# Kernel optimization log

Hardware: AMD Instinct MI355X
Metric: run time of the kernel (lower is better)

The kernel has to match this reference:

```python
import jax, jax.numpy as jnp
import numpy as np
from jax import lax

TAU = 2.0
V_TH = 1.0
V_RESET = 0.0
ALPHA = 2.0

@jax.custom_vjp
def atan_spike(u):
    # Heaviside forward, ATan surrogate backward
    return (u >= 0).astype(u.dtype)

def _atan_fwd(u):
    return atan_spike(u), u

def _atan_bwd(u, g):
    grad = (ALPHA / 2.0) / (1.0 + (ALPHA * jnp.pi / 2.0 * u) ** 2)
    return (g * grad,)

atan_spike.defvjp(_atan_fwd, _atan_bwd)


def setup_inputs() -> dict:
    key = jax.random.key(0)
    k1, k2 = jax.random.split(key)
    T, B, C_in, H, Wd = 8, 16, 64, 64, 64
    C_out = 128
    x = jax.random.normal(k1, (T, B, C_in, H, Wd), dtype=jnp.float32)
    # kaiming-like scale for 3x3 conv
    W = jax.random.normal(k2, (C_out, C_in, 3, 3), dtype=jnp.float32) * (1.0 / np.sqrt(C_in * 9))
    return {"x": x, "W": W}


def reference(x, W):
    T, B, C_in, H, Wd = x.shape
    C_out = W.shape[0]
    # conv over flattened (T*B) batch, 3x3, padding=1, no bias
    z = lax.conv_general_dilated(
        x.reshape(T * B, C_in, H, Wd), W,
        window_strides=(1, 1), padding="SAME",
        dimension_numbers=("NCHW", "OIHW", "NCHW"))
    z = z.reshape(T, B, C_out, H, Wd)

    def step(v, xt):
        # v_reset = 0: v += (x - v) / tau
        v = v + (xt - (v - V_RESET)) / TAU
        s = atan_spike(v - V_TH)
        v = v * (1.0 - s) + V_RESET * s
        return v, s

    _, spikes = lax.scan(step, jnp.zeros_like(z[0]), z)
    return spikes  # [T, B, C_out, H, W]
```

## Files before the change

### kernel.cpp

```cpp
#include <hip/hip_runtime.h>

#define TT 8
#define BB 16
#define CIN 64
#define COUT 128
#define HH 64
#define WW 64

#define TILE_H 4
#define TILE_W 16
#define XS_H (TILE_H + 2)
#define XS_W (TILE_W + 2)
#define XS_ROW (XS_H * XS_W)
#define XS_N (CIN * XS_ROW)

__global__ __launch_bounds__(256, 2)
void convlif_f64(const float* __restrict__ x, const float* __restrict__ Wt,
                 float* __restrict__ out) {
    __shared__ double xs[XS_N];

    const int tid = threadIdx.x;
    const int pt = tid & 15;
    const int cg = tid >> 4;
    const int w0 = blockIdx.x * TILE_W;
    const int h0 = blockIdx.y * TILE_H;
    const int b = blockIdx.z;
    const int co_base = cg * 8;

    double v[32];
#pragma unroll
    for (int i = 0; i < 32; ++i) v[i] = 0.0;

    for (int t = 0; t < TT; ++t) {
        __syncthreads();
        const float* xb = x + (size_t)(t * BB + b) * (CIN * HH * WW);
        for (int idx = tid; idx < XS_N; idx += 256) {
            int ci = idx / XS_ROW;
            int rem = idx - ci * XS_ROW;
            int hh = rem / XS_W;
            int ww2 = rem - hh * XS_W;
            int gh = h0 - 1 + hh;
            int gw = w0 - 1 + ww2;
            double val = 0.0;
            if (gh >= 0 && gh < HH && gw >= 0 && gw < WW)
                val = (double)xb[ci * (HH * WW) + gh * WW + gw];
            xs[idx] = val;
        }
        __syncthreads();

        double acc[32];
#pragma unroll
        for (int i = 0; i < 32; ++i) acc[i] = 0.0;

        for (int ci = 0; ci < CIN; ++ci) {
            const float* wr = Wt + (size_t)co_base * (CIN * 9) + ci * 9;
            const double* xr = xs + ci * XS_ROW;
#pragma unroll
            for (int kh = 0; kh < 3; ++kh) {
#pragma unroll
                for (int kw = 0; kw < 3; ++kw) {
                    double wv[8];
#pragma unroll
                    for (int i = 0; i < 8; ++i)
                        wv[i] = (double)wr[i * (CIN * 9) + kh * 3 + kw];
                    double xv[4];
#pragma unroll
                    for (int j = 0; j < 4; ++j)
                        xv[j] = xr[(j + kh) * XS_W + pt + kw];
#pragma unroll
                    for (int i = 0; i < 8; ++i) {
#pragma unroll
                        for (int j = 0; j < 4; ++j)
                            acc[i * 4 + j] = fma(wv[i], xv[j], acc[i * 4 + j]);
                    }
                }
            }
        }

        float* ob = out + (size_t)(t * BB + b) * (COUT * HH * WW);
#pragma unroll
        for (int i = 0; i < 8; ++i) {
#pragma unroll
            for (int j = 0; j < 4; ++j) {
                int k = i * 4 + j;
                double vv = v[k] + (acc[k] - v[k]) * 0.5;
                bool s = (vv >= 1.0);
                ob[(size_t)(co_base + i) * (HH * WW) + (h0 + j) * WW + (w0 + pt)]
                    = s ? 1.0f : 0.0f;
                v[k] = s ? 0.0 : vv;
            }
        }
    }
}

extern "C" void kernel_launch(void* const* d_in, const int* in_sizes, int n_in,
                              void* d_out, int out_size, void* d_ws, size_t ws_size,
                              hipStream_t stream) {
    const float* x = (const float*)d_in[0];
    const float* Wt = (const float*)d_in[1];
    float* out = (float*)d_out;
    dim3 grid(WW / TILE_W, HH / TILE_H, BB);
    convlif_f64<<<grid, 256, 0, stream>>>(x, Wt, out);
}
```

Measured before the change: 2.271 ms.

## Pre-convert weights to transposed fp64 and chunk input channels in LDS

A new prepass kernel converts the fp32 weights into an fp64 array in the workspace, transposed so the 8 output channels a thread needs are contiguous and can be read as double2 vector loads. Per-FMA float-to-double conversion and strided weight loads are removed. The input-channel loop is split into chunks of 32, which halves the LDS tile so three blocks can fit per CU (launch bounds raised to 3). This adds an extra kernel launch and two more barriers per timestep. The old kernel is kept as a fallback for when the workspace is too small.

Result: slower. 3.437 ms (+51.3%).

```diff
diff --git a/kernel.cpp b/kernel.cpp
--- a/kernel.cpp
+++ b/kernel.cpp
@@ -12,11 +12,25 @@
 #define XS_H (TILE_H + 2)
 #define XS_W (TILE_W + 2)
 #define XS_ROW (XS_H * XS_W)
-#define XS_N (CIN * XS_ROW)
-
-__global__ __launch_bounds__(256, 2)
-void convlif_f64(const float* __restrict__ x, const float* __restrict__ Wt,
-                 float* __restrict__ out) {
+#define CI_CHUNK 32
+#define XS_N (CI_CHUNK * XS_ROW)
+
+#define W_ELEMS (CIN * 9 * COUT)
+#define W_BYTES (W_ELEMS * 8)
+
+__global__ void wconv_f64(const float* __restrict__ Wt, double* __restrict__ wd) {
+    int idx = blockIdx.x * 256 + threadIdx.x;
+    if (idx >= W_ELEMS) return;
+    int co = idx & 127;
+    int cik = idx >> 7;
+    int ci = cik / 9;
+    int k = cik - ci * 9;
+    wd[idx] = (double)Wt[((size_t)co * CIN + ci) * 9 + k];
+}
+
+__global__ __launch_bounds__(256, 3)
+void convlif_f64w(const float* __restrict__ x, const double* __restrict__ wd,
+                  float* __restrict__ out) {
     __shared__ double xs[XS_N];
 
     const int tid = threadIdx.x;
@@ -32,37 +46,37 @@
     for (int i = 0; i < 32; ++i) v[i] = 0.0;
 
     for (int t = 0; t < TT; ++t) {
-        __syncthreads();
         const float* xb = x + (size_t)(t * BB + b) * (CIN * HH * WW);
-        for (int idx = tid; idx < XS_N; idx += 256) {
-            int ci = idx / XS_ROW;
-            int rem = idx - ci * XS_ROW;
-            int hh = rem / XS_W;
-            int ww2 = rem - hh * XS_W;
-            int gh = h0 - 1 + hh;
-            int gw = w0 - 1 + ww2;
-            double val = 0.0;
-            if (gh >= 0 && gh < HH && gw >= 0 && gw < WW)
-                val = (double)xb[ci * (HH * WW) + gh * WW + gw];
-            xs[idx] = val;
-        }
-        __syncthreads();
-
         double acc[32];
 #pragma unroll
         for (int i = 0; i < 32; ++i) acc[i] = 0.0;
 
-        for (int ci = 0; ci < CIN; ++ci) {
-            const float* wr = Wt + (size_t)co_base * (CIN * 9) + ci * 9;
-            const double* xr = xs + ci * XS_ROW;
-#pragma unroll
-            for (int kh = 0; kh < 3; ++kh) {
-#pragma unroll
-                for (int kw = 0; kw < 3; ++kw) {
-                    double wv[8];
-#pragma unroll
-                    for (int i = 0; i < 8; ++i)
-                        wv[i] = (double)wr[i * (CIN * 9) + kh * 3 + kw];
+        for (int cc = 0; cc < CIN; cc += CI_CHUNK) {
+            __syncthreads();
+            for (int idx = tid; idx < XS_N; idx += 256) {
+                int cil = idx / XS_ROW;
+                int rem = idx - cil * XS_ROW;
+                int hh = rem / XS_W;
+                int ww2 = rem - hh * XS_W;
+                int gh = h0 - 1 + hh;
+                int gw = w0 - 1 + ww2;
+                double val = 0.0;
+                if (gh >= 0 && gh < HH && gw >= 0 && gw < WW)
+                    val = (double)xb[(cc + cil) * (HH * WW) + gh * WW + gw];
+                xs[idx] = val;
+            }
+            __syncthreads();
+
+            for (int cil = 0; cil < CI_CHUNK; ++cil) {
+                const double* xr = xs + cil * XS_ROW;
+                const double* wrow = wd + (size_t)((cc + cil) * 9) * COUT + co_base;
+#pragma unroll
+                for (int k = 0; k < 9; ++k) {
+                    const int kh = k / 3, kw = k - kh * 3;
+                    const double2* wp = (const double2*)(wrow + k * COUT);
+                    double2 w01 = wp[0], w23 = wp[1], w45 = wp[2], w67 = wp[3];
+                    double wv[8] = {w01.x, w01.y, w23.x, w23.y,
+                                    w45.x, w45.y, w67.x, w67.y};
                     double xv[4];
 #pragma unroll
                     for (int j = 0; j < 4; ++j)
@@ -93,6 +107,83 @@
     }
 }
 
+#define FXS_H 6
+#define FXS_W 18
+#define FXS_ROW (FXS_H * FXS_W)
+#define FXS_N (CIN * FXS_ROW)
+__global__ __launch_bounds__(256, 2)
+void convlif_f64(const float* __restrict__ x, const float* __restrict__ Wt,
+                 float* __restrict__ out) {
+    __shared__ double xs[FXS_N];
+    const int tid = threadIdx.x;
+    const int pt = tid & 15;
+    const int cg = tid >> 4;
+    const int w0 = blockIdx.x * TILE_W;
+    const int h0 = blockIdx.y * TILE_H;
+    const int b = blockIdx.z;
+    const int co_base = cg * 8;
+    double v[32];
+#pragma unroll
+    for (int i = 0; i < 32; ++i) v[i] = 0.0;
+    for (int t = 0; t < TT; ++t) {
+        __syncthreads();
+        const float* xb = x + (size_t)(t * BB + b) * (CIN * HH * WW);
+        for (int idx = tid; idx < FXS_N; idx += 256) {
+            int ci = idx / FXS_ROW;
+            int rem = idx - ci * FXS_ROW;
+            int hh = rem / FXS_W;
+            int ww2 = rem - hh * FXS_W;
+            int gh = h0 - 1 + hh;
+            int gw = w0 - 1 + ww2;
+            double val = 0.0;
+            if (gh >= 0 && gh < HH && gw >= 0 && gw < WW)
+                val = (double)xb[ci * (HH * WW) + gh * WW + gw];
+            xs[idx] = val;
+        }
+        __syncthreads();
+        double acc[32];
+#pragma unroll
+        for (int i = 0; i < 32; ++i) acc[i] = 0.0;
+        for (int ci = 0; ci < CIN; ++ci) {
+            const float* wr = Wt + (size_t)co_base * (CIN * 9) + ci * 9;
+            const double* xr = xs + ci * FXS_ROW;
+#pragma unroll
+            for (int kh = 0; kh < 3; ++kh) {
+#pragma unroll
+                for (int kw = 0; kw < 3; ++kw) {
+                    double wv[8];
+#pragma unroll
+                    for (int i = 0; i < 8; ++i)
+                        wv[i] = (double)wr[i * (CIN * 9) + kh * 3 + kw];
+                    double xv[4];
+#pragma unroll
+                    for (int j = 0; j < 4; ++j)
+                        xv[j] = xr[(j + kh) * FXS_W + pt + kw];
+#pragma unroll
+                    for (int i = 0; i < 8; ++i) {
+#pragma unroll
+                        for (int j = 0; j < 4; ++j)
+                            acc[i * 4 + j] = fma(wv[i], xv[j], acc[i * 4 + j]);
+                    }
+                }
+            }
+        }
+        float* ob = out + (size_t)(t * BB + b) * (COUT * HH * WW);
+#pragma unroll
+        for (int i = 0; i < 8; ++i) {
+#pragma unroll
+            for (int j = 0; j < 4; ++j) {
+                int k = i * 4 + j;
+                double vv = v[k] + (acc[k] - v[k]) * 0.5;
+                bool s = (vv >= 1.0);
+                ob[(size_t)(co_base + i) * (HH * WW) + (h0 + j) * WW + (w0 + pt)]
+                    = s ? 1.0f : 0.0f;
+                v[k] = s ? 0.0 : vv;
+            }
+        }
+    }
+}
+
 extern "C" void kernel_launch(void* const* d_in, const int* in_sizes, int n_in,
                               void* d_out, int out_size, void* d_ws, size_t ws_size,
                               hipStream_t stream) {
@@ -100,5 +191,11 @@
     const float* Wt = (const float*)d_in[1];
     float* out = (float*)d_out;
     dim3 grid(WW / TILE_W, HH / TILE_H, BB);
-    convlif_f64<<<grid, 256, 0, stream>>>(x, Wt, out);
-}
+    if (ws_size >= (size_t)W_BYTES) {
+        double* wd = (double*)d_ws;
+        wconv_f64<<<(W_ELEMS + 255) / 256, 256, 0, stream>>>(Wt, wd);
+        convlif_f64w<<<grid, 256, 0, stream>>>(x, wd, out);
+    } else {
+        convlif_f64<<<grid, 256, 0, stream>>>(x, Wt, out);
+    }
+}
```
